# Performance work log

Measured on AMD Instinct MI355X. Metric: run time of the kernel, lower is better.

## Reference

```python
import jax, jax.numpy as jnp
import numpy as np

N, D, DFF, E, K = 2048, 1024, 4096, 8, 2  # tokens, d_model, d_ff, num_expert, top_k


def setup_inputs() -> dict:
    key = jax.random.key(0)
    ks = jax.random.split(key, 5)
    s = 0.02  # init scale
    return {
        "moe_inp": jax.random.normal(ks[0], (N, D), jnp.float32),
        "Wg": jax.random.normal(ks[1], (D, E), jnp.float32) * s,   # gate linear
        "bg": jnp.zeros((E,), jnp.float32),
        "W1": jax.random.normal(ks[2], (E, D, DFF), jnp.float32) * s,  # htoh4 per expert
        "b1": jnp.zeros((E, DFF), jnp.float32),
        "W2": jax.random.normal(ks[3], (E, DFF, D), jnp.float32) * s,  # h4toh per expert
        "b2": jnp.zeros((E, D), jnp.float32),
    }


def reference(moe_inp, Wg, bg, W1, b1, W2, b2):
    # --- NaiveGate: top-k experts per token, softmax over selected logits ---
    logits = moe_inp @ Wg + bg                      # [N, E]
    top_val, top_idx = jax.lax.top_k(logits, K)     # [N, K]
    score = jax.nn.softmax(top_val, axis=-1)        # [N, K]

    # Dense combine weights c[n, e] = sum_j score[n, j] * 1{top_idx[n, j] == e}.
    # This is the mathematically exact equivalent of scatter -> grouped expert
    # GEMM -> gather -> score-weighted combine in fmoe.
    comb = jnp.einsum(
        "nke,nk->ne", jax.nn.one_hot(top_idx, E, dtype=moe_inp.dtype), score
    )                                               # [N, E]

    # --- per-expert FFN: relu(x W1 + b1) W2 + b2, masked-combined by comb ---
    h = jax.nn.relu(jnp.einsum("nd,edh->enh", moe_inp, W1) + b1[:, None, :])  # [E, N, DFF]
    out = jnp.einsum("enh,ehd,ne->nd", h, W2, comb) + comb @ b2               # [N, D]
    return out
```

## Files before the change

### kernel.cpp

```cpp
#include <hip/hip_runtime.h>
#include <hip/hip_bf16.h>
#include <cstdint>
#include <cstddef>

#define NTOKS  2048
#define DMODEL 1024
#define DFFN   4096
#define NEXP   8
#define TSLOTS 40

typedef __attribute__((ext_vector_type(8))) short short8;
typedef __attribute__((ext_vector_type(4))) float f32x4;
typedef __attribute__((ext_vector_type(4))) unsigned short u16x4;
typedef __attribute__((ext_vector_type(8))) unsigned short u16x8;

static constexpr size_t alignup(size_t x) { return (x + 255) & ~(size_t)255; }
static constexpr size_t OFF_XB   = 0;
static constexpr size_t OFF_CNT  = alignup(OFF_XB + (size_t)(NTOKS + 1) * DMODEL * 2);
static constexpr size_t OFF_OFFS = OFF_CNT + 256;
static constexpr size_t OFF_TOKE = OFF_OFFS + 256;
static constexpr size_t OFF_TOKT = OFF_TOKE + (size_t)NTOKS * 2 * 4;
static constexpr size_t OFF_TOKS = OFF_TOKT + (size_t)NTOKS * 2 * 4;
static constexpr size_t OFF_TI   = alignup(OFF_TOKS + (size_t)NTOKS * 2 * 4);
static constexpr size_t OFF_CAP  = alignup(OFF_TI + 512);
static constexpr size_t OFF_H    = alignup(OFF_CAP + (size_t)NEXP * NTOKS * 4);
static constexpr size_t OFF_Y    = alignup(OFF_H + (size_t)(NTOKS * 2 + 128) * DFFN * 2);
static constexpr size_t OFF_WB   = alignup(OFF_Y + (size_t)2 * NTOKS * 2 * DMODEL * 4);

__device__ inline unsigned short f2bf(float f) {
  __hip_bfloat16 h = __float2bfloat16(f);
  return __builtin_bit_cast(unsigned short, h);
}

__device__ inline void gload16(const void* g, void* l) {
  __builtin_amdgcn_global_load_lds((const __attribute__((address_space(1))) unsigned int*)g,
                                   (__attribute__((address_space(3))) unsigned int*)l, 16, 0, 0);
}

__global__ __launch_bounds__(256) void k_convert(const float* __restrict__ x,
                                                 unsigned short* __restrict__ xb,
                                                 int* __restrict__ cnt) {
  if (blockIdx.x == 0 && threadIdx.x < NEXP) cnt[threadIdx.x] = 0;
  size_t base = ((size_t)blockIdx.x * 256 + threadIdx.x) * 8;
  const size_t total = (size_t)(NTOKS + 1) * DMODEL;
  if (base >= total) return;
  u16x8 o;
  if (base < (size_t)NTOKS * DMODEL) {
    f32x4 a = *(const f32x4*)(x + base);
    f32x4 b = *(const f32x4*)(x + base + 4);
#pragma unroll
    for (int j = 0; j < 4; ++j) { o[j] = f2bf(a[j]); o[4 + j] = f2bf(b[j]); }
  } else {
#pragma unroll
    for (int j = 0; j < 8; ++j) o[j] = 0;
  }
  *(u16x8*)(xb + base) = o;
}

template <int R, int C>
__global__ __launch_bounds__(256) void k_transconv(const float* __restrict__ W,
                                                   unsigned short* __restrict__ WT) {
  __shared__ unsigned short T[64][66];
  const int e = blockIdx.z;
  const int c0 = blockIdx.x * 64, r0 = blockIdx.y * 64;
  const float* Wp = W + (size_t)e * R * C;
  unsigned short* Tp = WT + (size_t)e * R * C;
  const int tid = threadIdx.x;
  const int rr = tid >> 4, cc = (tid & 15) << 2;
#pragma unroll
  for (int i = 0; i < 4; ++i) {
    int r = rr + (i << 4);
    f32x4 v = *(const f32x4*)(Wp + (size_t)(r0 + r) * C + c0 + cc);
    T[r][cc]     = f2bf(v[0]);
    T[r][cc + 1] = f2bf(v[1]);
    T[r][cc + 2] = f2bf(v[2]);
    T[r][cc + 3] = f2bf(v[3]);
  }
  __syncthreads();
  const int c = tid >> 2, kc = (tid & 3) << 4;
  u16x8 o0, o1;
#pragma unroll
  for (int i = 0; i < 8; ++i) { o0[i] = T[kc + i][c]; o1[i] = T[kc + 8 + i][c]; }
  unsigned short* dst = Tp + (size_t)(c0 + c) * R + r0 + kc;
  *(u16x8*)(dst) = o0;
  *(u16x8*)(dst + 8) = o1;
}

__global__ __launch_bounds__(256) void k_gate(const float* __restrict__ x,
                                              const float* __restrict__ Wg,
                                              const float* __restrict__ bg,
                                              int* __restrict__ cnt,
                                              int* __restrict__ tok_e,
                                              int* __restrict__ tok_t,
                                              float* __restrict__ tok_s,
                                              int* __restrict__ cap) {
  const int w = threadIdx.x >> 6, lane = threadIdx.x & 63;
  const int n = blockIdx.x * 4 + w;
  float acc[8];
#pragma unroll
  for (int e = 0; e < 8; ++e) acc[e] = 0.f;
  const float* xr = x + (size_t)n * DMODEL;
#pragma unroll 4
  for (int it = 0; it < DMODEL / 64; ++it) {
    int d = it * 64 + lane;
    float xv = xr[d];
    f32x4 w0 = *(const f32x4*)(Wg + d * 8);
    f32x4 w1 = *(const f32x4*)(Wg + d * 8 + 4);
#pragma unroll
    for (int j = 0; j < 4; ++j) { acc[j] += xv * w0[j]; acc[4 + j] += xv * w1[j]; }
  }
#pragma unroll
  for (int e = 0; e < 8; ++e)
#pragma unroll
    for (int off = 32; off; off >>= 1) acc[e] += __shfl_xor(acc[e], off, 64);
  if (lane == 0) {
    float l[8];
#pragma unroll
    for (int e = 0; e < 8; ++e) l[e] = acc[e] + bg[e];
    int i0 = 0; float v0 = l[0];
#pragma unroll
    for (int e = 1; e < 8; ++e) if (l[e] > v0) { v0 = l[e]; i0 = e; }
    int i1 = (i0 == 0) ? 1 : 0; float v1 = l[i1];
#pragma unroll
    for (int e = 0; e < 8; ++e) if (e != i0 && l[e] > v1) { v1 = l[e]; i1 = e; }
    float t = expf(v1 - v0);
    float inv = 1.f / (1.f + t);
    float s0 = inv, s1 = t * inv;
    int t0 = atomicAdd(&cnt[i0], 1);
    int t1 = atomicAdd(&cnt[i1], 1);
    cap[i0 * NTOKS + t0] = n;
    cap[i1 * NTOKS + t1] = n;
    tok_e[2 * n] = i0; tok_e[2 * n + 1] = i1;
    tok_t[2 * n] = t0; tok_t[2 * n + 1] = t1;
    tok_s[2 * n] = s0; tok_s[2 * n + 1] = s1;
  }
}

__global__ void k_scan(const int* __restrict__ cnt, int* __restrict__ offs,
                       int2* __restrict__ tinfo) {
  if (threadIdx.x == 0) {
    int s = 0;
#pragma unroll
    for (int e = 0; e < NEXP; ++e) { offs[e] = s; s += cnt[e]; }
    int ns = 0;
    for (int e = 0; e < NEXP; ++e)
      for (int t = 0; t * 128 < cnt[e]; ++t) { tinfo[ns] = make_int2(e, t * 128); ++ns; }
    for (; ns < TSLOTS; ++ns) tinfo[ns] = make_int2(-1, 0);
  }
}

template <int KTOT, int NTOT, int BN, bool FIRST, int KSPLIT>
__global__ __launch_bounds__(256) void k_gemm(const unsigned short* __restrict__ Asrc,
                                              const unsigned short* __restrict__ Bsrc,
                                              const float* __restrict__ bias,
                                              const int* __restrict__ cnt,
                                              const int* __restrict__ offs,
                                              const int2* __restrict__ tinfo,
                                              const int* __restrict__ cap,
                                              unsigned short* __restrict__ hout,
                                              float* __restrict__ yout) {
  const int2 ti = tinfo[blockIdx.y];
  if (ti.x < 0) return;
  const int e = ti.x, t0 = ti.y;
  const int c = cnt[e];
  const int base = offs[e] + t0;
  const int n0 = blockIdx.x * BN;
  constexpr int KCH = KTOT / KSPLIT;
  constexpr int NT = KCH / 32;
  const int kb = blockIdx.z * KCH;

  const int tid = threadIdx.x, w = tid >> 6, lane = tid & 63;
  const int l15 = lane & 15, lq = lane >> 4;
  constexpr int MR = 4;
  constexpr int NR = BN / 32;
  constexpr int BR = BN / 64;
  const int wr = w >> 1, wc = w & 1;

  __shared__ unsigned short As[2][128 * 32];
  __shared__ unsigned short Bs[2][BN * 32];

  const int rl = tid >> 2;
  const int sw = (((tid & 3) ^ (rl & 3) ^ ((rl >> 2) & 3)) << 3);
  const unsigned short* aptr[2];
#pragma unroll
  for (int r = 0; r < 2; ++r) {
    int row = r * 64 + rl;
    size_t gr;
    if constexpr (FIRST) gr = (size_t)((t0 + row < c) ? cap[e * NTOKS + t0 + row] : NTOKS);
    else                 gr = (size_t)(base + row);
    aptr[r] = Asrc + gr * (size_t)KTOT + kb + sw;
  }
  const unsigned short* Be = Bsrc + (size_t)e * ((size_t)KTOT * NTOT);
  const unsigned short* bptr[BR];
#pragma unroll
  for (int r = 0; r < BR; ++r)
    bptr[r] = Be + (size_t)(n0 + r * 64 + rl) * KTOT + kb + sw;

  auto stageA = [&](int k0, int b) {
#pragma unroll
    for (int r = 0; r < 2; ++r)
      gload16(aptr[r] + k0, &As[b][(r * 64 + w * 16) << 5]);
  };
  auto stageB = [&](int k0, int b) {
#pragma unroll
    for (int r = 0; r < BR; ++r)
      gload16(bptr[r] + k0, &Bs[b][(r * 64 + w * 16) << 5]);
  };

  f32x4 acc[MR][NR] = {};

  stageA(0, 0);
  stageB(0, 0);
  __syncthreads();

  int buf = 0;
  for (int t = 0; t < NT; ++t) {
    const int nxt = buf ^ 1;
    if (t + 1 < NT) { stageA((t + 1) * 32, nxt); stageB((t + 1) * 32, nxt); }

    short8 a[MR], b[NR];
    const int sw0 = ((lq ^ (l15 & 3) ^ ((l15 >> 2) & 3)) << 3);
#pragma unroll
    for (int m = 0; m < MR; ++m)
      a[m] = *(const short8*)&As[buf][((wr * 64 + m * 16 + l15) << 5) + sw0];
#pragma unroll
    for (int nn = 0; nn < NR; ++nn)
      b[nn] = *(const short8*)&Bs[buf][((wc * (BN / 2) + nn * 16 + l15) << 5) + sw0];
#pragma unroll
    for (int m = 0; m < MR; ++m)
#pragma unroll
      for (int nn = 0; nn < NR; ++nn)
        acc[m][nn] = __builtin_amdgcn_mfma_f32_16x16x32_bf16(a[m], b[nn], acc[m][nn], 0, 0, 0);

    __syncthreads();
    buf = nxt;
  }

  if constexpr (FIRST) {
    const float* be = bias + (size_t)e * NTOT;
#pragma unroll
    for (int m = 0; m < MR; ++m) {
#pragma unroll
      for (int q2 = 0; q2 < 4; ++q2) {
        int row = wr * 64 + m * 16 + lq * 4 + q2;
        if (t0 + row < c) {
          unsigned short* hr = hout + (size_t)(base + row) * NTOT;
#pragma unroll
          for (int nn = 0; nn < NR; ++nn) {
            int col = n0 + wc * (BN / 2) + nn * 16 + l15;
            float v = acc[m][nn][q2] + be[col];
            v = v > 0.f ? v : 0.f;
            hr[col] = f2bf(v);
          }
        }
      }
    }
  } else {
    float* yz = yout + (size_t)blockIdx.z * NTOKS * 2 * DMODEL;
#pragma unroll
    for (int m = 0; m < MR; ++m) {
#pragma unroll
      for (int q2 = 0; q2 < 4; ++q2) {
        int row = wr * 64 + m * 16 + lq * 4 + q2;
        if (t0 + row < c) {
          float* yr = yz + (size_t)(base + row) * NTOT;
#pragma unroll
          for (int nn = 0; nn < NR; ++nn) {
            int col = n0 + wc * (BN / 2) + nn * 16 + l15;
            yr[col] = acc[m][nn][q2];
          }
        }
      }
    }
  }
}

__global__ __launch_bounds__(256) void k_combine(const float* __restrict__ y,
                                                 const float* __restrict__ b2,
                                                 const int* __restrict__ tok_e,
                                                 const int* __restrict__ tok_t,
                                                 const float* __restrict__ tok_s,
                                                 const int* __restrict__ offs,
                                                 float* __restrict__ out) {
  const int n = blockIdx.x, t = threadIdx.x;
  const float* y1 = y + (size_t)NTOKS * 2 * DMODEL;
  const int e0 = tok_e[2 * n], e1 = tok_e[2 * n + 1];
  const int s0i = offs[e0] + tok_t[2 * n];
  const int s1i = offs[e1] + tok_t[2 * n + 1];
  const float sc0 = tok_s[2 * n], sc1 = tok_s[2 * n + 1];
  f32x4 v0 = *(const f32x4*)(y + (size_t)s0i * DMODEL + t * 4);
  f32x4 u0 = *(const f32x4*)(y1 + (size_t)s0i * DMODEL + t * 4);
  f32x4 v1 = *(const f32x4*)(y + (size_t)s1i * DMODEL + t * 4);
  f32x4 u1 = *(const f32x4*)(y1 + (size_t)s1i * DMODEL + t * 4);
  f32x4 c0 = *(const f32x4*)(b2 + (size_t)e0 * DMODEL + t * 4);
  f32x4 c1 = *(const f32x4*)(b2 + (size_t)e1 * DMODEL + t * 4);
  f32x4 r = sc0 * ((v0 + u0) + c0) + sc1 * ((v1 + u1) + c1);
  *(f32x4*)(out + (size_t)n * DMODEL + t * 4) = r;
}

extern "C" void kernel_launch(void* const* d_in, const int* in_sizes, int n_in,
                              void* d_out, int out_size, void* d_ws, size_t ws_size,
                              hipStream_t stream) {
  const float* x  = (const float*)d_in[0];
  const float* Wg = (const float*)d_in[1];
  const float* bg = (const float*)d_in[2];
  const float* W1 = (const float*)d_in[3];
  const float* b1 = (const float*)d_in[4];
  const float* W2 = (const float*)d_in[5];
  const float* b2 = (const float*)d_in[6];
  float* out = (float*)d_out;

  char* ws = (char*)d_ws;
  unsigned short* xb = (unsigned short*)(ws + OFF_XB);
  int*   cnt   = (int*)(ws + OFF_CNT);
  int*   offs  = (int*)(ws + OFF_OFFS);
  int*   tok_e = (int*)(ws + OFF_TOKE);
  int*   tok_t = (int*)(ws + OFF_TOKT);
  float* tok_s = (float*)(ws + OFF_TOKS);
  int2*  tinfo = (int2*)(ws + OFF_TI);
  int*   cap   = (int*)(ws + OFF_CAP);
  unsigned short* h  = (unsigned short*)(ws + OFF_H);
  float* y = (float*)(ws + OFF_Y);
  unsigned short* wb = (unsigned short*)(ws + OFF_WB);

  const int convBlocks = (int)(((size_t)(NTOKS + 1) * DMODEL / 8 + 255) / 256);
  k_convert<<<convBlocks, 256, 0, stream>>>(x, xb, cnt);
  k_gate<<<NTOKS / 4, 256, 0, stream>>>(x, Wg, bg, cnt, tok_e, tok_t, tok_s, cap);
  k_scan<<<1, 64, 0, stream>>>(cnt, offs, tinfo);

  k_transconv<DMODEL, DFFN><<<dim3(DFFN / 64, DMODEL / 64, NEXP), 256, 0, stream>>>(W1, wb);
  k_gemm<DMODEL, DFFN, 128, true, 1><<<dim3(DFFN / 128, TSLOTS, 1), 256, 0, stream>>>(
      xb, wb, b1, cnt, offs, tinfo, cap, h, nullptr);

  k_transconv<DFFN, DMODEL><<<dim3(DMODEL / 64, DFFN / 64, NEXP), 256, 0, stream>>>(W2, wb);
  k_gemm<DFFN, DMODEL, 64, false, 2><<<dim3(DMODEL / 64, TSLOTS, 2), 256, 0, stream>>>(
      h, wb, nullptr, cnt, offs, tinfo, cap, nullptr, y);

  k_combine<<<NTOKS, 256, 0, stream>>>(y, b2, tok_e, tok_t, tok_s, offs, out);
}
```

Measured before the change: 282.6 us.

## Fuse fp32 weight transpose and bf16 conversion into GEMM B-tile loading

Drops the separate transpose-convert kernels for W1 and W2. Each GEMM now reads fp32 weights directly from global memory into registers, converts them to bf16 and writes them transposed and swizzled into shared memory. The register prefetch overlaps with the MFMA work. This removes a full write and re-read of the weights. The cost is that each GEMM reads fp32 weights, twice the bytes of bf16, and re-reads them for every token tile of an expert. The B tile also moves through VGPRs and scattered shared-memory stores instead of the direct global-to-LDS load.

```diff
diff --git a/kernel.cpp b/kernel.cpp
--- a/kernel.cpp
+++ b/kernel.cpp
@@ -25,7 +25,6 @@
 static constexpr size_t OFF_CAP  = alignup(OFF_TI + 512);
 static constexpr size_t OFF_H    = alignup(OFF_CAP + (size_t)NEXP * NTOKS * 4);
 static constexpr size_t OFF_Y    = alignup(OFF_H + (size_t)(NTOKS * 2 + 128) * DFFN * 2);
-static constexpr size_t OFF_WB   = alignup(OFF_Y + (size_t)2 * NTOKS * 2 * DMODEL * 4);
 
 __device__ inline unsigned short f2bf(float f) {
   __hip_bfloat16 h = __float2bfloat16(f);
@@ -57,35 +56,6 @@
   *(u16x8*)(xb + base) = o;
 }
 
-template <int R, int C>
-__global__ __launch_bounds__(256) void k_transconv(const float* __restrict__ W,
-                                                   unsigned short* __restrict__ WT) {
-  __shared__ unsigned short T[64][66];
-  const int e = blockIdx.z;
-  const int c0 = blockIdx.x * 64, r0 = blockIdx.y * 64;
-  const float* Wp = W + (size_t)e * R * C;
-  unsigned short* Tp = WT + (size_t)e * R * C;
-  const int tid = threadIdx.x;
-  const int rr = tid >> 4, cc = (tid & 15) << 2;
-#pragma unroll
-  for (int i = 0; i < 4; ++i) {
-    int r = rr + (i << 4);
-    f32x4 v = *(const f32x4*)(Wp + (size_t)(r0 + r) * C + c0 + cc);
-    T[r][cc]     = f2bf(v[0]);
-    T[r][cc + 1] = f2bf(v[1]);
-    T[r][cc + 2] = f2bf(v[2]);
-    T[r][cc + 3] = f2bf(v[3]);
-  }
-  __syncthreads();
-  const int c = tid >> 2, kc = (tid & 3) << 4;
-  u16x8 o0, o1;
-#pragma unroll
-  for (int i = 0; i < 8; ++i) { o0[i] = T[kc + i][c]; o1[i] = T[kc + 8 + i][c]; }
-  unsigned short* dst = Tp + (size_t)(c0 + c) * R + r0 + kc;
-  *(u16x8*)(dst) = o0;
-  *(u16x8*)(dst + 8) = o1;
-}
-
 __global__ __launch_bounds__(256) void k_gate(const float* __restrict__ x,
                                               const float* __restrict__ Wg,
                                               const float* __restrict__ bg,
@@ -151,7 +121,7 @@
 
 template <int KTOT, int NTOT, int BN, bool FIRST, int KSPLIT>
 __global__ __launch_bounds__(256) void k_gemm(const unsigned short* __restrict__ Asrc,
-                                              const unsigned short* __restrict__ Bsrc,
+                                              const float* __restrict__ Wsrc,
                                               const float* __restrict__ bias,
                                               const int* __restrict__ cnt,
                                               const int* __restrict__ offs,
@@ -173,7 +143,6 @@
   const int l15 = lane & 15, lq = lane >> 4;
   constexpr int MR = 4;
   constexpr int NR = BN / 32;
-  constexpr int BR = BN / 64;
   const int wr = w >> 1, wc = w & 1;
 
   __shared__ unsigned short As[2][128 * 32];
@@ -190,33 +159,55 @@
     else                 gr = (size_t)(base + row);
     aptr[r] = Asrc + gr * (size_t)KTOT + kb + sw;
   }
-  const unsigned short* Be = Bsrc + (size_t)e * ((size_t)KTOT * NTOT);
-  const unsigned short* bptr[BR];
-#pragma unroll
-  for (int r = 0; r < BR; ++r)
-    bptr[r] = Be + (size_t)(n0 + r * 64 + rl) * KTOT + kb + sw;
-
   auto stageA = [&](int k0, int b) {
 #pragma unroll
     for (int r = 0; r < 2; ++r)
       gload16(aptr[r] + k0, &As[b][(r * 64 + w * 16) << 5]);
   };
-  auto stageB = [&](int k0, int b) {
-#pragma unroll
-    for (int r = 0; r < BR; ++r)
-      gload16(bptr[r] + k0, &Bs[b][(r * 64 + w * 16) << 5]);
+
+  const float* We = Wsrc + (size_t)e * ((size_t)KTOT * NTOT);
+  constexpr bool BACT128 = (BN == 64);
+  const bool bact = !BACT128 || (tid < 128);
+  const int tcB = BACT128 ? (tid & 15) : (tid & 31);
+  const int trB = BACT128 ? (tid >> 4) : (tid >> 5);
+  const float* bcol = We + n0 + (tcB << 2);
+
+  auto loadB = [&](int k0, f32x4* bv) {
+    if (bact) {
+      const float* bp = bcol + (size_t)(kb + k0 + trB * 4) * NTOT;
+#pragma unroll
+      for (int i = 0; i < 4; ++i) bv[i] = *(const f32x4*)(bp + (size_t)i * NTOT);
+    }
   };
+  auto writeB = [&](const f32x4* bv, int b) {
+    if (bact) {
+#pragma unroll
+      for (int j = 0; j < 4; ++j) {
+        const int col = (tcB << 2) + j;
+        const int x = (col ^ (col >> 2)) & 3;
+        const int slot = (((trB >> 1) ^ x) << 1) + (trB & 1);
+        u16x4 p = { f2bf(bv[0][j]), f2bf(bv[1][j]), f2bf(bv[2][j]), f2bf(bv[3][j]) };
+        *(u16x4*)&Bs[b][(col << 5) + (slot << 2)] = p;
+      }
+    }
+  };
 
   f32x4 acc[MR][NR] = {};
 
-  stageA(0, 0);
-  stageB(0, 0);
+  {
+    f32x4 bv[4];
+    stageA(0, 0);
+    loadB(0, bv);
+    writeB(bv, 0);
+  }
   __syncthreads();
 
   int buf = 0;
   for (int t = 0; t < NT; ++t) {
     const int nxt = buf ^ 1;
-    if (t + 1 < NT) { stageA((t + 1) * 32, nxt); stageB((t + 1) * 32, nxt); }
+    const bool pre = (t + 1 < NT);
+    f32x4 bv[4];
+    if (pre) { stageA((t + 1) * 32, nxt); loadB((t + 1) * 32, bv); }
 
     short8 a[MR], b[NR];
     const int sw0 = ((lq ^ (l15 & 3) ^ ((l15 >> 2) & 3)) << 3);
@@ -232,6 +223,7 @@
       for (int nn = 0; nn < NR; ++nn)
         acc[m][nn] = __builtin_amdgcn_mfma_f32_16x16x32_bf16(a[m], b[nn], acc[m][nn], 0, 0, 0);
 
+    if (pre) writeB(bv, nxt);
     __syncthreads();
     buf = nxt;
   }
@@ -321,20 +313,17 @@
   int*   cap   = (int*)(ws + OFF_CAP);
   unsigned short* h  = (unsigned short*)(ws + OFF_H);
   float* y = (float*)(ws + OFF_Y);
-  unsigned short* wb = (unsigned short*)(ws + OFF_WB);
 
   const int convBlocks = (int)(((size_t)(NTOKS + 1) * DMODEL / 8 + 255) / 256);
   k_convert<<<convBlocks, 256, 0, stream>>>(x, xb, cnt);
   k_gate<<<NTOKS / 4, 256, 0, stream>>>(x, Wg, bg, cnt, tok_e, tok_t, tok_s, cap);
   k_scan<<<1, 64, 0, stream>>>(cnt, offs, tinfo);
 
-  k_transconv<DMODEL, DFFN><<<dim3(DFFN / 64, DMODEL / 64, NEXP), 256, 0, stream>>>(W1, wb);
   k_gemm<DMODEL, DFFN, 128, true, 1><<<dim3(DFFN / 128, TSLOTS, 1), 256, 0, stream>>>(
-      xb, wb, b1, cnt, offs, tinfo, cap, h, nullptr);
-
-  k_transconv<DFFN, DMODEL><<<dim3(DMODEL / 64, DFFN / 64, NEXP), 256, 0, stream>>>(W2, wb);
+      xb, W1, b1, cnt, offs, tinfo, cap, h, nullptr);
+
   k_gemm<DFFN, DMODEL, 64, false, 2><<<dim3(DMODEL / 64, TSLOTS, 2), 256, 0, stream>>>(
-      h, wb, nullptr, cnt, offs, tinfo, cap, nullptr, y);
+      h, W2, nullptr, cnt, offs, tinfo, cap, nullptr, y);
 
   k_combine<<<NTOKS, 256, 0, stream>>>(y, b2, tok_e, tok_t, tok_s, offs, out);
 }
```

Result: no change. 284.2 us (+0.6%).

## Enlarge grouped expert GEMM tiles to 256 rows with 512-thread blocks and K=64 steps

Applied to the files above, without the earlier changes.

The grouped expert GEMMs now use 256-token M tiles (tile slots built in steps of 256), 8 waves per block, wider N tiles (256 for the first GEMM, 128 for the second), and a 64-wide K step. Each K step issues two MFMA passes from LDS, and the LDS swizzle is updated to an 8-way XOR. The aim is more operand reuse per byte loaded and fewer barriers per unit of work. The cost is far fewer blocks (for example 16x24 for GEMM1), more padding waste on partially filled expert tiles, and heavier register and LDS pressure (64KB+ LDS per block), all of which can reduce occupancy.

```diff
diff --git a/kernel.cpp b/kernel.cpp
--- a/kernel.cpp
+++ b/kernel.cpp
@@ -7,7 +7,7 @@
 #define DMODEL 1024
 #define DFFN   4096
 #define NEXP   8
-#define TSLOTS 40
+#define TSLOTS 24
 
 typedef __attribute__((ext_vector_type(8))) short short8;
 typedef __attribute__((ext_vector_type(4))) float f32x4;
@@ -24,7 +24,7 @@
 static constexpr size_t OFF_TI   = alignup(OFF_TOKS + (size_t)NTOKS * 2 * 4);
 static constexpr size_t OFF_CAP  = alignup(OFF_TI + 512);
 static constexpr size_t OFF_H    = alignup(OFF_CAP + (size_t)NEXP * NTOKS * 4);
-static constexpr size_t OFF_Y    = alignup(OFF_H + (size_t)(NTOKS * 2 + 128) * DFFN * 2);
+static constexpr size_t OFF_Y    = alignup(OFF_H + (size_t)(NTOKS * 2 + 256) * DFFN * 2);
 static constexpr size_t OFF_WB   = alignup(OFF_Y + (size_t)2 * NTOKS * 2 * DMODEL * 4);
 
 __device__ inline unsigned short f2bf(float f) {
@@ -144,21 +144,21 @@
     for (int e = 0; e < NEXP; ++e) { offs[e] = s; s += cnt[e]; }
     int ns = 0;
     for (int e = 0; e < NEXP; ++e)
-      for (int t = 0; t * 128 < cnt[e]; ++t) { tinfo[ns] = make_int2(e, t * 128); ++ns; }
+      for (int t = 0; t * 256 < cnt[e]; ++t) { tinfo[ns] = make_int2(e, t * 256); ++ns; }
     for (; ns < TSLOTS; ++ns) tinfo[ns] = make_int2(-1, 0);
   }
 }
 
 template <int KTOT, int NTOT, int BN, bool FIRST, int KSPLIT>
-__global__ __launch_bounds__(256) void k_gemm(const unsigned short* __restrict__ Asrc,
-                                              const unsigned short* __restrict__ Bsrc,
-                                              const float* __restrict__ bias,
-                                              const int* __restrict__ cnt,
-                                              const int* __restrict__ offs,
-                                              const int2* __restrict__ tinfo,
-                                              const int* __restrict__ cap,
-                                              unsigned short* __restrict__ hout,
-                                              float* __restrict__ yout) {
+__global__ __launch_bounds__(512, 2) void k_gemm(const unsigned short* __restrict__ Asrc,
+                                                 const unsigned short* __restrict__ Bsrc,
+                                                 const float* __restrict__ bias,
+                                                 const int* __restrict__ cnt,
+                                                 const int* __restrict__ offs,
+                                                 const int2* __restrict__ tinfo,
+                                                 const int* __restrict__ cap,
+                                                 unsigned short* __restrict__ hout,
+                                                 float* __restrict__ yout) {
   const int2 ti = tinfo[blockIdx.y];
   if (ti.x < 0) return;
   const int e = ti.x, t0 = ti.y;
@@ -166,24 +166,25 @@
   const int base = offs[e] + t0;
   const int n0 = blockIdx.x * BN;
   constexpr int KCH = KTOT / KSPLIT;
-  constexpr int NT = KCH / 32;
+  constexpr int NT = KCH / 64;
   const int kb = blockIdx.z * KCH;
 
   const int tid = threadIdx.x, w = tid >> 6, lane = tid & 63;
   const int l15 = lane & 15, lq = lane >> 4;
-  constexpr int MR = 4;
-  constexpr int NR = BN / 32;
+  constexpr int MR = 8;
+  constexpr int WN = BN / 4;
+  constexpr int NR = WN / 16;
   constexpr int BR = BN / 64;
-  const int wr = w >> 1, wc = w & 1;
-
-  __shared__ unsigned short As[2][128 * 32];
-  __shared__ unsigned short Bs[2][BN * 32];
-
-  const int rl = tid >> 2;
-  const int sw = (((tid & 3) ^ (rl & 3) ^ ((rl >> 2) & 3)) << 3);
-  const unsigned short* aptr[2];
-#pragma unroll
-  for (int r = 0; r < 2; ++r) {
+  const int wr = w >> 2, wc = w & 3;
+
+  __shared__ unsigned short As[2][256 * 64];
+  __shared__ unsigned short Bs[2][BN * 64];
+
+  const int rl = tid >> 3;
+  const int sw = ((tid & 7) ^ (rl & 7)) << 3;
+  const unsigned short* aptr[4];
+#pragma unroll
+  for (int r = 0; r < 4; ++r) {
     int row = r * 64 + rl;
     size_t gr;
     if constexpr (FIRST) gr = (size_t)((t0 + row < c) ? cap[e * NTOKS + t0 + row] : NTOKS);
@@ -198,13 +199,13 @@
 
   auto stageA = [&](int k0, int b) {
 #pragma unroll
-    for (int r = 0; r < 2; ++r)
-      gload16(aptr[r] + k0, &As[b][(r * 64 + w * 16) << 5]);
+    for (int r = 0; r < 4; ++r)
+      gload16(aptr[r] + k0, &As[b][(r * 64 + (w << 3)) << 6]);
   };
   auto stageB = [&](int k0, int b) {
 #pragma unroll
     for (int r = 0; r < BR; ++r)
-      gload16(bptr[r] + k0, &Bs[b][(r * 64 + w * 16) << 5]);
+      gload16(bptr[r] + k0, &Bs[b][(r * 64 + (w << 3)) << 6]);
   };
 
   f32x4 acc[MR][NR] = {};
@@ -216,21 +217,32 @@
   int buf = 0;
   for (int t = 0; t < NT; ++t) {
     const int nxt = buf ^ 1;
-    if (t + 1 < NT) { stageA((t + 1) * 32, nxt); stageB((t + 1) * 32, nxt); }
-
+    if (t + 1 < NT) { stageA((t + 1) << 6, nxt); stageB((t + 1) << 6, nxt); }
+
+    const int sw0 = (lq ^ (l15 & 7)) << 3;
     short8 a[MR], b[NR];
-    const int sw0 = ((lq ^ (l15 & 3) ^ ((l15 >> 2) & 3)) << 3);
 #pragma unroll
     for (int m = 0; m < MR; ++m)
-      a[m] = *(const short8*)&As[buf][((wr * 64 + m * 16 + l15) << 5) + sw0];
+      a[m] = *(const short8*)&As[buf][((wr * 128 + m * 16 + l15) << 6) + sw0];
 #pragma unroll
     for (int nn = 0; nn < NR; ++nn)
-      b[nn] = *(const short8*)&Bs[buf][((wc * (BN / 2) + nn * 16 + l15) << 5) + sw0];
+      b[nn] = *(const short8*)&Bs[buf][((wc * WN + nn * 16 + l15) << 6) + sw0];
 #pragma unroll
     for (int m = 0; m < MR; ++m)
 #pragma unroll
       for (int nn = 0; nn < NR; ++nn)
         acc[m][nn] = __builtin_amdgcn_mfma_f32_16x16x32_bf16(a[m], b[nn], acc[m][nn], 0, 0, 0);
+#pragma unroll
+    for (int m = 0; m < MR; ++m)
+      a[m] = *(const short8*)&As[buf][((wr * 128 + m * 16 + l15) << 6) + (sw0 ^ 32)];
+#pragma unroll
+    for (int nn = 0; nn < NR; ++nn)
+      b[nn] = *(const short8*)&Bs[buf][((wc * WN + nn * 16 + l15) << 6) + (sw0 ^ 32)];
+#pragma unroll
+    for (int m = 0; m < MR; ++m)
+#pragma unroll
+      for (int nn = 0; nn < NR; ++nn)
+        acc[m][nn] = __builtin_amdgcn_mfma_f32_16x16x32_bf16(a[m], b[nn], acc[m][nn], 0, 0, 0);
 
     __syncthreads();
     buf = nxt;
@@ -242,12 +254,12 @@
     for (int m = 0; m < MR; ++m) {
 #pragma unroll
       for (int q2 = 0; q2 < 4; ++q2) {
-        int row = wr * 64 + m * 16 + lq * 4 + q2;
+        int row = wr * 128 + m * 16 + lq * 4 + q2;
         if (t0 + row < c) {
           unsigned short* hr = hout + (size_t)(base + row) * NTOT;
 #pragma unroll
           for (int nn = 0; nn < NR; ++nn) {
-            int col = n0 + wc * (BN / 2) + nn * 16 + l15;
+            int col = n0 + wc * WN + nn * 16 + l15;
             float v = acc[m][nn][q2] + be[col];
             v = v > 0.f ? v : 0.f;
             hr[col] = f2bf(v);
@@ -261,12 +273,12 @@
     for (int m = 0; m < MR; ++m) {
 #pragma unroll
       for (int q2 = 0; q2 < 4; ++q2) {
-        int row = wr * 64 + m * 16 + lq * 4 + q2;
+        int row = wr * 128 + m * 16 + lq * 4 + q2;
         if (t0 + row < c) {
           float* yr = yz + (size_t)(base + row) * NTOT;
 #pragma unroll
           for (int nn = 0; nn < NR; ++nn) {
-            int col = n0 + wc * (BN / 2) + nn * 16 + l15;
+            int col = n0 + wc * WN + nn * 16 + l15;
             yr[col] = acc[m][nn][q2];
           }
         }
@@ -329,11 +341,11 @@
   k_scan<<<1, 64, 0, stream>>>(cnt, offs, tinfo);
 
   k_transconv<DMODEL, DFFN><<<dim3(DFFN / 64, DMODEL / 64, NEXP), 256, 0, stream>>>(W1, wb);
-  k_gemm<DMODEL, DFFN, 128, true, 1><<<dim3(DFFN / 128, TSLOTS, 1), 256, 0, stream>>>(
+  k_gemm<DMODEL, DFFN, 256, true, 1><<<dim3(DFFN / 256, TSLOTS, 1), 512, 0, stream>>>(
       xb, wb, b1, cnt, offs, tinfo, cap, h, nullptr);
 
   k_transconv<DFFN, DMODEL><<<dim3(DMODEL / 64, DFFN / 64, NEXP), 256, 0, stream>>>(W2, wb);
-  k_gemm<DFFN, DMODEL, 64, false, 2><<<dim3(DMODEL / 64, TSLOTS, 2), 256, 0, stream>>>(
+  k_gemm<DFFN, DMODEL, 128, false, 2><<<dim3(DMODEL / 128, TSLOTS, 2), 512, 0, stream>>>(
       h, wb, nullptr, cnt, offs, tinfo, cap, nullptr, y);
 
   k_combine<<<NTOKS, 256, 0, stream>>>(y, b2, tok_e, tok_t, tok_s, offs, out);
```

After: 314.3 us. 1.11x slower.

## Add 256x256-tile 8-wave GEMM kernel for first expert FFN layer

Applied to the files above, without the earlier changes.

Replaces the first grouped GEMM (x·W1 with ReLU) with a new 512-thread kernel that computes 256x256 output tiles using double-buffered LDS loads and phased MFMA execution, using s_setprio around the MFMA blocks. The scan now builds two tile lists, one with 256-token slots for the new kernel and one with 128-token slots for the unchanged second GEMM. Larger tiles raise arithmetic intensity and cut redundant global loads. The cost is more padding waste per expert and fewer blocks (16x24), which may underfill the GPU's compute units. The LDS footprint is 128 KB per block and the h workspace padding is enlarged.

```diff
diff --git a/kernel.cpp b/kernel.cpp
--- a/kernel.cpp
+++ b/kernel.cpp
@@ -7,7 +7,8 @@
 #define DMODEL 1024
 #define DFFN   4096
 #define NEXP   8
-#define TSLOTS 40
+#define TS256  24
+#define TS128  40
 
 typedef __attribute__((ext_vector_type(8))) short short8;
 typedef __attribute__((ext_vector_type(4))) float f32x4;
@@ -22,9 +23,10 @@
 static constexpr size_t OFF_TOKT = OFF_TOKE + (size_t)NTOKS * 2 * 4;
 static constexpr size_t OFF_TOKS = OFF_TOKT + (size_t)NTOKS * 2 * 4;
 static constexpr size_t OFF_TI   = alignup(OFF_TOKS + (size_t)NTOKS * 2 * 4);
-static constexpr size_t OFF_CAP  = alignup(OFF_TI + 512);
+static constexpr size_t OFF_TI2  = OFF_TI + 256;
+static constexpr size_t OFF_CAP  = alignup(OFF_TI2 + TS128 * 8);
 static constexpr size_t OFF_H    = alignup(OFF_CAP + (size_t)NEXP * NTOKS * 4);
-static constexpr size_t OFF_Y    = alignup(OFF_H + (size_t)(NTOKS * 2 + 128) * DFFN * 2);
+static constexpr size_t OFF_Y    = alignup(OFF_H + (size_t)(NTOKS * 2 + 256) * DFFN * 2);
 static constexpr size_t OFF_WB   = alignup(OFF_Y + (size_t)2 * NTOKS * 2 * DMODEL * 4);
 
 __device__ inline unsigned short f2bf(float f) {
@@ -137,15 +139,159 @@
 }
 
 __global__ void k_scan(const int* __restrict__ cnt, int* __restrict__ offs,
-                       int2* __restrict__ tinfo) {
+                       int2* __restrict__ ti256, int2* __restrict__ ti128) {
   if (threadIdx.x == 0) {
     int s = 0;
 #pragma unroll
     for (int e = 0; e < NEXP; ++e) { offs[e] = s; s += cnt[e]; }
-    int ns = 0;
+    int a = 0;
     for (int e = 0; e < NEXP; ++e)
-      for (int t = 0; t * 128 < cnt[e]; ++t) { tinfo[ns] = make_int2(e, t * 128); ++ns; }
-    for (; ns < TSLOTS; ++ns) tinfo[ns] = make_int2(-1, 0);
+      for (int t = 0; t * 256 < cnt[e]; ++t) { ti256[a] = make_int2(e, t * 256); ++a; }
+    for (; a < TS256; ++a) ti256[a] = make_int2(-1, 0);
+    int b = 0;
+    for (int e = 0; e < NEXP; ++e)
+      for (int t = 0; t * 128 < cnt[e]; ++t) { ti128[b] = make_int2(e, t * 128); ++b; }
+    for (; b < TS128; ++b) ti128[b] = make_int2(-1, 0);
+  }
+}
+
+__global__ __launch_bounds__(512, 2) void k_gemm8(const unsigned short* __restrict__ Asrc,
+                                                  const unsigned short* __restrict__ Bsrc,
+                                                  const float* __restrict__ bias,
+                                                  const int* __restrict__ cnt,
+                                                  const int* __restrict__ offs,
+                                                  const int2* __restrict__ tinfo,
+                                                  const int* __restrict__ cap,
+                                                  unsigned short* __restrict__ hout) {
+  constexpr int KTOT = DMODEL, NTOT = DFFN;
+  constexpr int NTILES = KTOT / 64;
+  constexpr int NI = NTILES / 2;
+  const int2 ti = tinfo[blockIdx.y];
+  if (ti.x < 0) return;
+  const int e = ti.x, t0 = ti.y;
+  const int c = cnt[e];
+  const int base = offs[e] + t0;
+  const int n0 = blockIdx.x * 256;
+
+  const int tid = threadIdx.x, w = tid >> 6, lane = tid & 63;
+  const int l15 = lane & 15, lq = lane >> 4;
+  const int wr = w >> 2, wc = w & 3;
+
+  __shared__ unsigned short As[2][256 * 64];
+  __shared__ unsigned short Bs[2][256 * 64];
+
+  const int rl = tid >> 3;
+  const int sw = ((tid & 7) ^ (rl & 7)) << 3;
+  const unsigned short* aptr[4];
+#pragma unroll
+  for (int r = 0; r < 4; ++r) {
+    int row = r * 64 + rl;
+    size_t gr = (size_t)((t0 + row < c) ? cap[e * NTOKS + t0 + row] : NTOKS);
+    aptr[r] = Asrc + gr * (size_t)KTOT + sw;
+  }
+  const unsigned short* Be = Bsrc + (size_t)e * ((size_t)KTOT * NTOT);
+  const unsigned short* bptr[4];
+#pragma unroll
+  for (int r = 0; r < 4; ++r)
+    bptr[r] = Be + (size_t)(n0 + r * 64 + rl) * KTOT + sw;
+
+  auto stage_tile = [&](int tl) {
+    const int b = tl & 1;
+    const int k0 = tl << 6;
+#pragma unroll
+    for (int r = 0; r < 4; ++r)
+      gload16(aptr[r] + k0, &As[b][(r * 64 + (w << 3)) << 6]);
+#pragma unroll
+    for (int r = 0; r < 4; ++r)
+      gload16(bptr[r] + k0, &Bs[b][(r * 64 + (w << 3)) << 6]);
+  };
+
+  f32x4 acc[8][4] = {};
+  short8 alo[4], ahi[4];
+  const int sw0 = (lq ^ (l15 & 7)) << 3;
+
+  stage_tile(0);
+  asm volatile("s_waitcnt vmcnt(0)" ::: "memory");
+  __builtin_amdgcn_s_barrier();
+  asm volatile("" ::: "memory");
+
+#define PHASE(BUF, MH, NH)                                                          \
+  {                                                                                 \
+    if ((NH) == 0) {                                                                \
+      _Pragma("unroll")                                                             \
+      for (int mm = 0; mm < 4; ++mm) {                                              \
+        const unsigned short* ab =                                                  \
+            &As[BUF][((wr * 128 + (MH) * 64 + mm * 16 + l15) << 6)];                \
+        alo[mm] = *(const short8*)&ab[sw0];                                         \
+        ahi[mm] = *(const short8*)&ab[sw0 ^ 32];                                    \
+      }                                                                             \
+    }                                                                               \
+    short8 blo[2], bhi[2];                                                          \
+    _Pragma("unroll")                                                               \
+    for (int nn = 0; nn < 2; ++nn) {                                                \
+      const unsigned short* bb =                                                    \
+          &Bs[BUF][((wc * 64 + (NH) * 32 + nn * 16 + l15) << 6)];                   \
+      blo[nn] = *(const short8*)&bb[sw0];                                           \
+      bhi[nn] = *(const short8*)&bb[sw0 ^ 32];                                      \
+    }                                                                               \
+    asm volatile("" ::: "memory");                                                  \
+    __builtin_amdgcn_s_setprio(1);                                                  \
+    _Pragma("unroll")                                                               \
+    for (int mm = 0; mm < 4; ++mm)                                                  \
+      _Pragma("unroll")                                                             \
+      for (int nn = 0; nn < 2; ++nn) {                                              \
+        acc[(MH) * 4 + mm][(NH) * 2 + nn] =                                         \
+            __builtin_amdgcn_mfma_f32_16x16x32_bf16(                                \
+                alo[mm], blo[nn], acc[(MH) * 4 + mm][(NH) * 2 + nn], 0, 0, 0);      \
+        acc[(MH) * 4 + mm][(NH) * 2 + nn] =                                         \
+            __builtin_amdgcn_mfma_f32_16x16x32_bf16(                                \
+                ahi[mm], bhi[nn], acc[(MH) * 4 + mm][(NH) * 2 + nn], 0, 0, 0);      \
+      }                                                                             \
+    __builtin_amdgcn_s_setprio(0);                                                  \
+  }
+#define FENCE_BAR                                                                   \
+  asm volatile("" ::: "memory");                                                    \
+  __builtin_amdgcn_s_barrier();                                                     \
+  asm volatile("" ::: "memory");
+#define DRAIN_BAR                                                                   \
+  asm volatile("s_waitcnt vmcnt(0)" ::: "memory");                                  \
+  __builtin_amdgcn_s_barrier();                                                     \
+  asm volatile("" ::: "memory");
+
+  for (int i = 0; i < NI; ++i) {
+    const int t2 = 2 * i;
+    stage_tile(t2 + 1);
+    PHASE(0, 0, 0) FENCE_BAR
+    PHASE(0, 0, 1) FENCE_BAR
+    PHASE(0, 1, 0) FENCE_BAR
+    PHASE(0, 1, 1) DRAIN_BAR
+    if (i + 1 < NI) stage_tile(t2 + 2);
+    PHASE(1, 0, 0) FENCE_BAR
+    PHASE(1, 0, 1) FENCE_BAR
+    PHASE(1, 1, 0) FENCE_BAR
+    PHASE(1, 1, 1) DRAIN_BAR
+  }
+#undef PHASE
+#undef FENCE_BAR
+#undef DRAIN_BAR
+
+  const float* be = bias + (size_t)e * NTOT;
+#pragma unroll
+  for (int m = 0; m < 8; ++m) {
+#pragma unroll
+    for (int q2 = 0; q2 < 4; ++q2) {
+      int row = wr * 128 + m * 16 + lq * 4 + q2;
+      if (t0 + row < c) {
+        unsigned short* hr = hout + (size_t)(base + row) * NTOT;
+#pragma unroll
+        for (int nn = 0; nn < 4; ++nn) {
+          int col = n0 + wc * 64 + nn * 16 + l15;
+          float v = acc[m][nn][q2] + be[col];
+          v = v > 0.f ? v : 0.f;
+          hr[col] = f2bf(v);
+        }
+      }
+    }
   }
 }
 
@@ -317,7 +463,8 @@
   int*   tok_e = (int*)(ws + OFF_TOKE);
   int*   tok_t = (int*)(ws + OFF_TOKT);
   float* tok_s = (float*)(ws + OFF_TOKS);
-  int2*  tinfo = (int2*)(ws + OFF_TI);
+  int2*  ti256 = (int2*)(ws + OFF_TI);
+  int2*  ti128 = (int2*)(ws + OFF_TI2);
   int*   cap   = (int*)(ws + OFF_CAP);
   unsigned short* h  = (unsigned short*)(ws + OFF_H);
   float* y = (float*)(ws + OFF_Y);
@@ -326,15 +473,15 @@
   const int convBlocks = (int)(((size_t)(NTOKS + 1) * DMODEL / 8 + 255) / 256);
   k_convert<<<convBlocks, 256, 0, stream>>>(x, xb, cnt);
   k_gate<<<NTOKS / 4, 256, 0, stream>>>(x, Wg, bg, cnt, tok_e, tok_t, tok_s, cap);
-  k_scan<<<1, 64, 0, stream>>>(cnt, offs, tinfo);
+  k_scan<<<1, 64, 0, stream>>>(cnt, offs, ti256, ti128);
 
   k_transconv<DMODEL, DFFN><<<dim3(DFFN / 64, DMODEL / 64, NEXP), 256, 0, stream>>>(W1, wb);
-  k_gemm<DMODEL, DFFN, 128, true, 1><<<dim3(DFFN / 128, TSLOTS, 1), 256, 0, stream>>>(
-      xb, wb, b1, cnt, offs, tinfo, cap, h, nullptr);
+  k_gemm8<<<dim3(DFFN / 256, TS256), 512, 0, stream>>>(
+      xb, wb, b1, cnt, offs, ti256, cap, h);
 
   k_transconv<DFFN, DMODEL><<<dim3(DMODEL / 64, DFFN / 64, NEXP), 256, 0, stream>>>(W2, wb);
-  k_gemm<DFFN, DMODEL, 64, false, 2><<<dim3(DMODEL / 64, TSLOTS, 2), 256, 0, stream>>>(
-      h, wb, nullptr, cnt, offs, tinfo, cap, nullptr, y);
+  k_gemm<DFFN, DMODEL, 64, false, 2><<<dim3(DMODEL / 64, TS128, 2), 256, 0, stream>>>(
+      h, wb, nullptr, cnt, offs, ti128, cap, nullptr, y);
 
   k_combine<<<NTOKS, 256, 0, stream>>>(y, b2, tok_e, tok_t, tok_s, offs, out);
 }
```

After: 291.2 us. 1.03x slower.
